# Kernel optimization log

Hardware: AMD Instinct MI355X
Metric: run time of the kernel (lower is better)

Reference implementation:

```python
import jax, jax.numpy as jnp
import numpy as np

N_LAYERS = 2
N_ENT = 50000


def setup_inputs() -> dict:
    key = jax.random.key(0)
    k1, k2, k3, k4, k5 = jax.random.split(key, 5)
    R, N, D, E = 16, N_ENT, 128, 50000
    return {
        "ent_emb": jax.random.normal(k1, (N, D), dtype=jnp.float32),
        "rel_trans": jax.random.normal(k2, (R, D, D), dtype=jnp.float32) * (1.0 / np.sqrt(D)),
        "edge_val": jax.random.uniform(k3, (R, E), dtype=jnp.float32),
        "edge_row": jax.random.randint(k4, (R, E), 0, N, dtype=jnp.int32),
        "edge_col": jax.random.randint(k5, (R, E), 0, N, dtype=jnp.int32),
    }


def _spmm(row, col, val, emb):
    # out[i] = sum_{edges e with row[e]==i} val[e] * emb[col[e]]  (A @ emb)
    msgs = emb[col] * val[:, None]            # [E, d]
    return jax.ops.segment_sum(msgs, row, num_segments=N_ENT)  # [N, d]


def reference(ent_emb, rel_trans, edge_val, edge_row, edge_col):
    emb = ent_emb
    for _ in range(N_LAYERS):
        # per-relation sparse A_r @ emb -> [R, N, d]
        emb_acc = jax.vmap(_spmm, in_axes=(0, 0, 0, None))(edge_row, edge_col, edge_val, emb)
        # batched relation transform: rel_trans[r] @ emb_acc[r].T, transposed back
        tmp = jnp.einsum("rij,rnj->rni", rel_trans, emb_acc)  # [R, N, d]
        emb = jax.nn.relu(jnp.sum(tmp, axis=0))               # [N, d]
    # F.normalize: L2 along dim=1 with eps=1e-12
    norm = jnp.linalg.norm(emb, axis=1, keepdims=True)
    emb = emb / jnp.maximum(norm, 1e-12)
    return emb
```

## Files before the change

### kernel.cpp

```cpp
#include <hip/hip_runtime.h>
#include <stdint.h>

#define NE 50000
#define DD 128
#define RR 16
#define EE 50000
#define NT 32
#define NTOT (RR * NE)
#define SCAN_BLK 4096
#define NSCAN ((NTOT + SCAN_BLK - 1) / SCAN_BLK)

typedef short  shortx8 __attribute__((ext_vector_type(8)));
typedef short  shortx4 __attribute__((ext_vector_type(4)));
typedef float  floatx4 __attribute__((ext_vector_type(4)));

__device__ __forceinline__ unsigned short f2bf(float f) {
    unsigned u = __float_as_uint(f);
    u += 0x7fffu + ((u >> 16) & 1u);
    return (unsigned short)(u >> 16);
}
__device__ __forceinline__ float bf2f(unsigned short h) {
    return __uint_as_float(((unsigned)h) << 16);
}

#define ZB 782
#define TB 128
#define EB 6250
__global__ void prep_k(const float* __restrict__ rt, unsigned short* __restrict__ Tf,
                       const float4* __restrict__ emb, shortx4* __restrict__ embA,
                       int* __restrict__ counts) {
    int b = blockIdx.x, t = threadIdx.x;
    if (b < ZB) {
        int i4 = b * 256 + t;
        if (i4 < NTOT / 4) *(int4*)(counts + i4 * 4) = make_int4(0, 0, 0, 0);
    } else if (b < ZB + TB) {
        int c = (b - ZB) * 256 + t;
        int r = c >> 11, row = (c >> 4) & 127, cb = c & 15;
        int kt = cb >> 2, qq = cb & 3, rg = row >> 4, m = row & 15;
        const float4* src = (const float4*)(rt + (size_t)c * 8);
        float4 v0 = src[0], v1 = src[1];
        shortx8 w;
        w[0] = (short)f2bf(v0.x); w[1] = (short)f2bf(v0.y);
        w[2] = (short)f2bf(v0.z); w[3] = (short)f2bf(v0.w);
        w[4] = (short)f2bf(v1.x); w[5] = (short)f2bf(v1.y);
        w[6] = (short)f2bf(v1.z); w[7] = (short)f2bf(v1.w);
        size_t idx = ((((size_t)r * 8 + rg) * 4 + kt) * 64 + qq * 16 + m) * 8;
        *(shortx8*)(Tf + idx) = w;
    } else {
        int i = (b - ZB - TB) * 256 + t;
        if (i < NE * DD / 4) {
            float4 v = emb[i];
            shortx4 w;
            w[0] = (short)f2bf(v.x); w[1] = (short)f2bf(v.y);
            w[2] = (short)f2bf(v.z); w[3] = (short)f2bf(v.w);
            embA[i] = w;
        }
    }
}

__global__ void hist_k(const int* __restrict__ erow, int* __restrict__ counts,
                       uchar4* __restrict__ rank) {
    int r  = blockIdx.y;
    int i4 = blockIdx.x * 256 + threadIdx.x;
    if (i4 < EE / 4) {
        int4 rw = *(const int4*)(erow + (size_t)r * EE + i4 * 4);
        uchar4 rk;
        rk.x = (unsigned char)atomicAdd(&counts[rw.x * RR + r], 1);
        rk.y = (unsigned char)atomicAdd(&counts[rw.y * RR + r], 1);
        rk.z = (unsigned char)atomicAdd(&counts[rw.z * RR + r], 1);
        rk.w = (unsigned char)atomicAdd(&counts[rw.w * RR + r], 1);
        rank[(size_t)r * (EE / 4) + i4] = rk;
    }
}

__global__ void scanA(const int* __restrict__ c, int* __restrict__ bsum) {
    int b = blockIdx.x, t = threadIdx.x;
    int base = b * SCAN_BLK + t * 16;
    int s = 0;
    #pragma unroll
    for (int i = 0; i < 16; i++) {
        int idx = base + i;
        if (idx < NTOT) s += c[idx];
    }
    __shared__ int sh[256];
    sh[t] = s;
    __syncthreads();
    for (int off = 128; off > 0; off >>= 1) {
        if (t < off) sh[t] += sh[t + off];
        __syncthreads();
    }
    if (t == 0) bsum[b] = sh[0];
}

__global__ void scanC(const int* __restrict__ counts, int* __restrict__ rp,
                      const int* __restrict__ bsum) {
    int b = blockIdx.x, t = threadIdx.x;
    __shared__ int shb[256];
    shb[t] = (t < NSCAN) ? bsum[t] : 0;
    __syncthreads();
    for (int off = 1; off < 256; off <<= 1) {
        int add = (t >= off) ? shb[t - off] : 0;
        __syncthreads();
        shb[t] += add;
        __syncthreads();
    }
    int blockPrefix = (b > 0) ? shb[b - 1] : 0;
    int base = b * SCAN_BLK + t * 16;
    int vals[16];
    int s = 0;
    #pragma unroll
    for (int i = 0; i < 16; i++) {
        int idx = base + i;
        vals[i] = (idx < NTOT) ? counts[idx] : 0;
        s += vals[i];
    }
    __shared__ int sh[256];
    sh[t] = s;
    __syncthreads();
    for (int off = 1; off < 256; off <<= 1) {
        int add = (t >= off) ? sh[t - off] : 0;
        __syncthreads();
        sh[t] += add;
        __syncthreads();
    }
    int run = blockPrefix + sh[t] - s;
    #pragma unroll
    for (int i = 0; i < 16; i++) {
        int idx = base + i;
        if (idx < NTOT) {
            rp[idx] = run;
            run += vals[i];
            if (idx == NTOT - 1) rp[NTOT] = run;
        }
    }
}

__global__ void fill_k(const int* __restrict__ erow, const int* __restrict__ ecol,
                       const float* __restrict__ eval, const int* __restrict__ rp,
                       const uchar4* __restrict__ rank, int2* __restrict__ edges) {
    int r  = blockIdx.y;
    int i4 = blockIdx.x * 256 + threadIdx.x;
    if (i4 < EE / 4) {
        int4   rw = *(const int4*)(erow + (size_t)r * EE + i4 * 4);
        int4   cl = *(const int4*)(ecol + (size_t)r * EE + i4 * 4);
        float4 vl = *(const float4*)(eval + (size_t)r * EE + i4 * 4);
        uchar4 rk = rank[(size_t)r * (EE / 4) + i4];
        edges[rp[rw.x * RR + r] + rk.x] = make_int2(cl.x, __float_as_int(vl.x));
        edges[rp[rw.y * RR + r] + rk.y] = make_int2(cl.y, __float_as_int(vl.y));
        edges[rp[rw.z * RR + r] + rk.z] = make_int2(cl.z, __float_as_int(vl.z));
        edges[rp[rw.w * RR + r] + rk.w] = make_int2(cl.w, __float_as_int(vl.w));
    }
}

__device__ __forceinline__ void accum_chunks(float a0[8], float a1[8], float v,
                                             shortx8 c0, shortx8 c1) {
    #pragma unroll
    for (int j = 0; j < 8; j++) {
        a0[j] = fmaf(v, bf2f((unsigned short)c0[j]), a0[j]);
        a1[j] = fmaf(v, bf2f((unsigned short)c1[j]), a1[j]);
    }
}

template<bool FINAL>
__global__ __launch_bounds__(256, 6)
void layer_k(const unsigned short* __restrict__ embIn,
             const unsigned short* __restrict__ Tf,
             const int* __restrict__ rp,
             const int2* __restrict__ eg,
             unsigned short* __restrict__ embOut,
             float* __restrict__ outF)
{
    __shared__ __align__(16) unsigned short Bt[32 * 128];
    __shared__ float ssred[4][32];

    const int t    = threadIdx.x;
    const int lane = t & 63;
    const int w    = t >> 6;
    const int colq = lane & 15;
    const int q    = lane >> 4;
    const int n0   = blockIdx.x * NT;
    const int nsub = t >> 3;
    const int dgrp = t & 7;

    floatx4 acc[2][2];
    #pragma unroll
    for (int a = 0; a < 2; a++)
        #pragma unroll
        for (int c = 0; c < 2; c++)
            acc[a][c] = (floatx4){0.f, 0.f, 0.f, 0.f};

    #pragma unroll 1
    for (int r = 0; r < RR; r++) {
        int n = n0 + nsub;
        bool ok = n < NE;
        int key = (ok ? n : 0) * RR + r;
        int a = rp[key], b2 = rp[key + 1];
        int s_ = a, c_ = ok ? (b2 - a) : 0;

        int2 E0 = eg[s_];
        int2 E1 = eg[s_ + 1];
        int   col0 = c_ > 0 ? E0.x : 0;
        int   col1 = c_ > 1 ? E1.x : 0;
        float v0_  = c_ > 0 ? __int_as_float(E0.y) : 0.f;
        float v1_  = c_ > 1 ? __int_as_float(E1.y) : 0.f;

        const unsigned short* r0 = embIn + (size_t)col0 * DD + dgrp * 8;
        const unsigned short* r1 = embIn + (size_t)col1 * DD + dgrp * 8;
        shortx8 m00 = *(const shortx8*)r0;
        shortx8 m01 = *(const shortx8*)(r0 + 64);
        shortx8 m10 = *(const shortx8*)r1;
        shortx8 m11 = *(const shortx8*)(r1 + 64);

        float a0[8], a1[8];
        #pragma unroll
        for (int j = 0; j < 8; j++) { a0[j] = 0.f; a1[j] = 0.f; }
        accum_chunks(a0, a1, v0_, m00, m01);
        accum_chunks(a0, a1, v1_, m10, m11);
        if (c_ > 2) {
            #pragma unroll 1
            for (int k = s_ + 2; k < s_ + c_; k++) {
                int2 E = eg[k];
                float v = __int_as_float(E.y);
                const unsigned short* rw_ = embIn + (size_t)E.x * DD + dgrp * 8;
                accum_chunks(a0, a1, v, *(const shortx8*)rw_, *(const shortx8*)(rw_ + 64));
            }
        }
        shortx8 w0, w1;
        #pragma unroll
        for (int j = 0; j < 8; j++) { w0[j] = (short)f2bf(a0[j]); w1[j] = (short)f2bf(a1[j]); }
        int pc = (dgrp ^ nsub) & 7;
        *(shortx8*)&Bt[nsub * 128 + pc * 8] = w0;
        *(shortx8*)&Bt[nsub * 128 + (8 | pc) * 8] = w1;
        __syncthreads();

        shortx8 afN[2];
        #pragma unroll
        for (int it2 = 0; it2 < 2; it2++)
            afN[it2] = *(const shortx8*)(Tf + ((((size_t)r * 8 + (w * 2 + it2)) * 4 + 0) * 64 + lane) * 8);
        #pragma unroll 1
        for (int kt = 0; kt < 4; kt++) {
            shortx8 afC[2];
            afC[0] = afN[0]; afC[1] = afN[1];
            if (kt < 3) {
                #pragma unroll
                for (int it2 = 0; it2 < 2; it2++)
                    afN[it2] = *(const shortx8*)(Tf + ((((size_t)r * 8 + (w * 2 + it2)) * 4 + (kt + 1)) * 64 + lane) * 8);
            }
            int lc = kt * 4 + q;
            shortx8 bfr[2];
            #pragma unroll
            for (int c = 0; c < 2; c++) {
                int nl = c * 16 + colq;
                int pcr = (lc & 8) | ((lc ^ nl) & 7);
                bfr[c] = *(const shortx8*)&Bt[nl * 128 + pcr * 8];
            }
            #pragma unroll
            for (int it2 = 0; it2 < 2; it2++)
                #pragma unroll
                for (int c = 0; c < 2; c++)
                    acc[it2][c] = __builtin_amdgcn_mfma_f32_16x16x32_bf16(afC[it2], bfr[c], acc[it2][c], 0, 0, 0);
        }
        __syncthreads();
    }

    if (!FINAL) {
        #pragma unroll
        for (int c = 0; c < 2; c++) {
            int n = n0 + c * 16 + colq;
            if (n < NE) {
                #pragma unroll
                for (int it2 = 0; it2 < 2; it2++) {
                    shortx4 wv;
                    #pragma unroll
                    for (int g = 0; g < 4; g++) {
                        float v = acc[it2][c][g];
                        v = v > 0.f ? v : 0.f;
                        wv[g] = (short)f2bf(v);
                    }
                    *(shortx4*)(embOut + ((size_t)n * DD + w * 32 + it2 * 16 + q * 4)) = wv;
                }
            }
        }
    } else {
        #pragma unroll
        for (int c = 0; c < 2; c++) {
            float ss = 0.f;
            #pragma unroll
            for (int it2 = 0; it2 < 2; it2++)
                #pragma unroll
                for (int g = 0; g < 4; g++) {
                    float v = acc[it2][c][g];
                    v = v > 0.f ? v : 0.f;
                    acc[it2][c][g] = v;
                    ss += v * v;
                }
            ss += __shfl_xor(ss, 16, 64);
            ss += __shfl_xor(ss, 32, 64);
            if (q == 0) ssred[w][c * 16 + colq] = ss;
        }
        __syncthreads();
        #pragma unroll
        for (int c = 0; c < 2; c++) {
            int nl = c * 16 + colq;
            float tot = ssred[0][nl] + ssred[1][nl] + ssred[2][nl] + ssred[3][nl];
            float scale = 1.f / fmaxf(sqrtf(tot), 1e-12f);
            int n = n0 + nl;
            if (n < NE) {
                #pragma unroll
                for (int it2 = 0; it2 < 2; it2++) {
                    floatx4 v4;
                    #pragma unroll
                    for (int g = 0; g < 4; g++) v4[g] = acc[it2][c][g] * scale;
                    *(floatx4*)(outF + ((size_t)n * DD + w * 32 + it2 * 16 + q * 4)) = v4;
                }
            }
        }
    }
}

static inline size_t align256(size_t x) { return (x + 255) & ~(size_t)255; }

extern "C" void kernel_launch(void* const* d_in, const int* in_sizes, int n_in,
                              void* d_out, int out_size, void* d_ws, size_t ws_size,
                              hipStream_t stream)
{
    const float* ent_emb   = (const float*)d_in[0];
    const float* rel_trans = (const float*)d_in[1];
    const float* edge_val  = (const float*)d_in[2];
    const int*   edge_row  = (const int*)d_in[3];
    const int*   edge_col  = (const int*)d_in[4];
    float* out = (float*)d_out;

    char* ws = (char*)d_ws;
    size_t off = 0;
    int* counts = (int*)(ws + off);  off = align256(off + (size_t)NTOT * 4);
    int* rpf    = (int*)(ws + off);  off = align256(off + ((size_t)NTOT + 1) * 4);
    int* bsum   = (int*)(ws + off);  off = align256(off + 256 * 4);
    uchar4* rank = (uchar4*)(ws + off); off = align256(off + (size_t)NTOT);
    int2* edges = (int2*)(ws + off); off = align256(off + ((size_t)NTOT + 4) * 8);
    unsigned short* Tf   = (unsigned short*)(ws + off); off = align256(off + (size_t)RR * DD * DD * 2);
    unsigned short* embA = (unsigned short*)(ws + off); off = align256(off + (size_t)NE * DD * 2);
    unsigned short* embB = (unsigned short*)(ws + off); off = align256(off + (size_t)NE * DD * 2);

    prep_k<<<ZB + TB + EB, 256, 0, stream>>>(rel_trans, Tf, (const float4*)ent_emb,
                                             (shortx4*)embA, counts);
    dim3 eg_grid((EE / 4 + 255) / 256, RR);
    hist_k<<<eg_grid, 256, 0, stream>>>(edge_row, counts, rank);
    scanA<<<NSCAN, 256, 0, stream>>>(counts, bsum);
    scanC<<<NSCAN, 256, 0, stream>>>(counts, rpf, bsum);
    fill_k<<<eg_grid, 256, 0, stream>>>(edge_row, edge_col, edge_val, rpf, rank, edges);

    int nb = (NE + NT - 1) / NT;
    layer_k<false><<<nb, 256, 0, stream>>>(embA, Tf, rpf, edges, embB, nullptr);
    layer_k<true ><<<nb, 256, 0, stream>>>(embB, Tf, rpf, edges, nullptr, out);
}
```

Before: 363.4 us.

## Switch CSR to relation-major order and gather edges per block via LDS atomics

The CSR key order changes from node-major to relation-major, so each block's edges for one relation form a single contiguous range. Each edge also carries its local node index packed into the upper bits of the column. The gather phase now spreads edges evenly across the 32 node slots, with one edge per 8-thread group, and accumulates into a float LDS tile using shared-memory atomics. This removes the load imbalance from per-node loops over uneven edge counts, but it adds LDS float atomics, a per-relation zeroing pass with an extra barrier, and a larger LDS footprint that may reduce occupancy.

```diff
diff --git a/kernel.cpp b/kernel.cpp
--- a/kernel.cpp
+++ b/kernel.cpp
@@ -64,11 +64,12 @@
     int i4 = blockIdx.x * 256 + threadIdx.x;
     if (i4 < EE / 4) {
         int4 rw = *(const int4*)(erow + (size_t)r * EE + i4 * 4);
+        int base0 = r * NE;
         uchar4 rk;
-        rk.x = (unsigned char)atomicAdd(&counts[rw.x * RR + r], 1);
-        rk.y = (unsigned char)atomicAdd(&counts[rw.y * RR + r], 1);
-        rk.z = (unsigned char)atomicAdd(&counts[rw.z * RR + r], 1);
-        rk.w = (unsigned char)atomicAdd(&counts[rw.w * RR + r], 1);
+        rk.x = (unsigned char)atomicAdd(&counts[base0 + rw.x], 1);
+        rk.y = (unsigned char)atomicAdd(&counts[base0 + rw.y], 1);
+        rk.z = (unsigned char)atomicAdd(&counts[base0 + rw.z], 1);
+        rk.w = (unsigned char)atomicAdd(&counts[base0 + rw.w], 1);
         rank[(size_t)r * (EE / 4) + i4] = rk;
     }
 }
@@ -145,19 +146,11 @@
         int4   cl = *(const int4*)(ecol + (size_t)r * EE + i4 * 4);
         float4 vl = *(const float4*)(eval + (size_t)r * EE + i4 * 4);
         uchar4 rk = rank[(size_t)r * (EE / 4) + i4];
-        edges[rp[rw.x * RR + r] + rk.x] = make_int2(cl.x, __float_as_int(vl.x));
-        edges[rp[rw.y * RR + r] + rk.y] = make_int2(cl.y, __float_as_int(vl.y));
-        edges[rp[rw.z * RR + r] + rk.z] = make_int2(cl.z, __float_as_int(vl.z));
-        edges[rp[rw.w * RR + r] + rk.w] = make_int2(cl.w, __float_as_int(vl.w));
-    }
-}
-
-__device__ __forceinline__ void accum_chunks(float a0[8], float a1[8], float v,
-                                             shortx8 c0, shortx8 c1) {
-    #pragma unroll
-    for (int j = 0; j < 8; j++) {
-        a0[j] = fmaf(v, bf2f((unsigned short)c0[j]), a0[j]);
-        a1[j] = fmaf(v, bf2f((unsigned short)c1[j]), a1[j]);
+        int base0 = r * NE;
+        edges[rp[base0 + rw.x] + rk.x] = make_int2(((rw.x & 31) << 17) | cl.x, __float_as_int(vl.x));
+        edges[rp[base0 + rw.y] + rk.y] = make_int2(((rw.y & 31) << 17) | cl.y, __float_as_int(vl.y));
+        edges[rp[base0 + rw.z] + rk.z] = make_int2(((rw.z & 31) << 17) | cl.z, __float_as_int(vl.z));
+        edges[rp[base0 + rw.w] + rk.w] = make_int2(((rw.w & 31) << 17) | cl.w, __float_as_int(vl.w));
     }
 }
 
@@ -170,6 +163,7 @@
              unsigned short* __restrict__ embOut,
              float* __restrict__ outF)
 {
+    __shared__ float BtF[32 * 132];
     __shared__ __align__(16) unsigned short Bt[32 * 128];
     __shared__ float ssred[4][32];
 
@@ -179,8 +173,9 @@
     const int colq = lane & 15;
     const int q    = lane >> 4;
     const int n0   = blockIdx.x * NT;
-    const int nsub = t >> 3;
+    const int node = t >> 3;
     const int dgrp = t & 7;
+    const int nhi  = (NE - n0 < NT) ? (NE - n0) : NT;
 
     floatx4 acc[2][2];
     #pragma unroll
@@ -191,46 +186,57 @@
 
     #pragma unroll 1
     for (int r = 0; r < RR; r++) {
-        int n = n0 + nsub;
-        bool ok = n < NE;
-        int key = (ok ? n : 0) * RR + r;
-        int a = rp[key], b2 = rp[key + 1];
-        int s_ = a, c_ = ok ? (b2 - a) : 0;
-
-        int2 E0 = eg[s_];
-        int2 E1 = eg[s_ + 1];
-        int   col0 = c_ > 0 ? E0.x : 0;
-        int   col1 = c_ > 1 ? E1.x : 0;
-        float v0_  = c_ > 0 ? __int_as_float(E0.y) : 0.f;
-        float v1_  = c_ > 1 ? __int_as_float(E1.y) : 0.f;
-
-        const unsigned short* r0 = embIn + (size_t)col0 * DD + dgrp * 8;
-        const unsigned short* r1 = embIn + (size_t)col1 * DD + dgrp * 8;
-        shortx8 m00 = *(const shortx8*)r0;
-        shortx8 m01 = *(const shortx8*)(r0 + 64);
-        shortx8 m10 = *(const shortx8*)r1;
-        shortx8 m11 = *(const shortx8*)(r1 + 64);
-
-        float a0[8], a1[8];
-        #pragma unroll
-        for (int j = 0; j < 8; j++) { a0[j] = 0.f; a1[j] = 0.f; }
-        accum_chunks(a0, a1, v0_, m00, m01);
-        accum_chunks(a0, a1, v1_, m10, m11);
-        if (c_ > 2) {
-            #pragma unroll 1
-            for (int k = s_ + 2; k < s_ + c_; k++) {
-                int2 E = eg[k];
-                float v = __int_as_float(E.y);
-                const unsigned short* rw_ = embIn + (size_t)E.x * DD + dgrp * 8;
-                accum_chunks(a0, a1, v, *(const shortx8*)rw_, *(const shortx8*)(rw_ + 64));
-            }
-        }
-        shortx8 w0, w1;
-        #pragma unroll
-        for (int j = 0; j < 8; j++) { w0[j] = (short)f2bf(a0[j]); w1[j] = (short)f2bf(a1[j]); }
-        int pc = (dgrp ^ nsub) & 7;
-        *(shortx8*)&Bt[nsub * 128 + pc * 8] = w0;
-        *(shortx8*)&Bt[nsub * 128 + (8 | pc) * 8] = w1;
+        #pragma unroll
+        for (int i = 0; i < 17; i++) {
+            int idx = t + i * 256;
+            if (idx < 32 * 132) BtF[idx] = 0.f;
+        }
+        __syncthreads();
+
+        int kb = r * NE + n0;
+        int lo = rp[kb];
+        int hi = rp[kb + nhi];
+        int ER = hi - lo;
+        #pragma unroll 1
+        for (int base = 0; base < ER; base += 32) {
+            int ei = base + node;
+            bool ok = ei < ER;
+            int2 E = eg[lo + ei];
+            int   x = ok ? E.x : 0;
+            float v = ok ? __int_as_float(E.y) : 0.f;
+            int nl  = (x >> 17) & 31;
+            int col = x & 0x1FFFF;
+            const unsigned short* rowp = embIn + (size_t)col * DD + dgrp * 16;
+            shortx8 c0 = *(const shortx8*)rowp;
+            shortx8 c1 = *(const shortx8*)(rowp + 8);
+            if (ok) {
+                float* dst = &BtF[nl * 132 + dgrp * 16];
+                #pragma unroll
+                for (int j = 0; j < 8; j++) atomicAdd(&dst[j],     v * bf2f((unsigned short)c0[j]));
+                #pragma unroll
+                for (int j = 0; j < 8; j++) atomicAdd(&dst[8 + j], v * bf2f((unsigned short)c1[j]));
+            }
+        }
+        __syncthreads();
+
+        {
+            const float* src = &BtF[node * 132 + dgrp * 8];
+            floatx4 f0 = *(const floatx4*)(src);
+            floatx4 f1 = *(const floatx4*)(src + 4);
+            floatx4 f2 = *(const floatx4*)(src + 64);
+            floatx4 f3 = *(const floatx4*)(src + 68);
+            shortx8 w0, w1;
+            #pragma unroll
+            for (int j = 0; j < 4; j++) {
+                w0[j]     = (short)f2bf(f0[j]);
+                w0[4 + j] = (short)f2bf(f1[j]);
+                w1[j]     = (short)f2bf(f2[j]);
+                w1[4 + j] = (short)f2bf(f3[j]);
+            }
+            int pc = (dgrp ^ node) & 7;
+            *(shortx8*)&Bt[node * 128 + pc * 8] = w0;
+            *(shortx8*)&Bt[node * 128 + (8 | pc) * 8] = w1;
+        }
         __syncthreads();
 
         shortx8 afN[2];
@@ -260,7 +266,6 @@
                 for (int c = 0; c < 2; c++)
                     acc[it2][c] = __builtin_amdgcn_mfma_f32_16x16x32_bf16(afC[it2], bfr[c], acc[it2][c], 0, 0, 0);
         }
-        __syncthreads();
     }
 
     if (!FINAL) {
@@ -282,6 +287,7 @@
             }
         }
     } else {
+        __syncthreads();
         #pragma unroll
         for (int c = 0; c < 2; c++) {
             float ss = 0.f;
@@ -337,7 +343,7 @@
     int* rpf    = (int*)(ws + off);  off = align256(off + ((size_t)NTOT + 1) * 4);
     int* bsum   = (int*)(ws + off);  off = align256(off + 256 * 4);
     uchar4* rank = (uchar4*)(ws + off); off = align256(off + (size_t)NTOT);
-    int2* edges = (int2*)(ws + off); off = align256(off + ((size_t)NTOT + 4) * 8);
+    int2* edges = (int2*)(ws + off); off = align256(off + ((size_t)NTOT + 32) * 8);
     unsigned short* Tf   = (unsigned short*)(ws + off); off = align256(off + (size_t)RR * DD * DD * 2);
     unsigned short* embA = (unsigned short*)(ws + off); off = align256(off + (size_t)NE * DD * 2);
     unsigned short* embB = (unsigned short*)(ws + off); off = align256(off + (size_t)NE * DD * 2);
```

Measured after the change: 1.440 ms. 3.96x slower.

## Double node tile to 64 with 512 threads and 8 waves per output slice

Applied to the files above, without the earlier changes.

Each block now handles 64 nodes with 512 threads, and each of 8 waves owns a 16-row slice of the output dimension instead of 4 waves with 32 rows. A wave loads one transform fragment per k-step and reuses it across four node column groups, so each fragment is loaded once per 64 nodes instead of once per 32. The edge loop also prefetches the next edge record one iteration ahead, and the edge buffer padding grows to cover that read past the end. Larger blocks halve the block count and raise per-block LDS and register demand, which may cut occupancy and lengthen the per-relation barriers.

```diff
diff --git a/kernel.cpp b/kernel.cpp
--- a/kernel.cpp
+++ b/kernel.cpp
@@ -5,7 +5,7 @@
 #define DD 128
 #define RR 16
 #define EE 50000
-#define NT 32
+#define NT 64
 #define NTOT (RR * NE)
 #define SCAN_BLK 4096
 #define NSCAN ((NTOT + SCAN_BLK - 1) / SCAN_BLK)
@@ -162,7 +162,7 @@
 }
 
 template<bool FINAL>
-__global__ __launch_bounds__(256, 6)
+__global__ __launch_bounds__(512, 6)
 void layer_k(const unsigned short* __restrict__ embIn,
              const unsigned short* __restrict__ Tf,
              const int* __restrict__ rp,
@@ -170,8 +170,8 @@
              unsigned short* __restrict__ embOut,
              float* __restrict__ outF)
 {
-    __shared__ __align__(16) unsigned short Bt[32 * 128];
-    __shared__ float ssred[4][32];
+    __shared__ __align__(16) unsigned short Bt[64 * 128];
+    __shared__ float ssred[8][64];
 
     const int t    = threadIdx.x;
     const int lane = t & 63;
@@ -182,12 +182,10 @@
     const int nsub = t >> 3;
     const int dgrp = t & 7;
 
-    floatx4 acc[2][2];
-    #pragma unroll
-    for (int a = 0; a < 2; a++)
-        #pragma unroll
-        for (int c = 0; c < 2; c++)
-            acc[a][c] = (floatx4){0.f, 0.f, 0.f, 0.f};
+    floatx4 acc[4];
+    #pragma unroll
+    for (int c = 0; c < 4; c++)
+        acc[c] = (floatx4){0.f, 0.f, 0.f, 0.f};
 
     #pragma unroll 1
     for (int r = 0; r < RR; r++) {
@@ -217,12 +215,14 @@
         accum_chunks(a0, a1, v0_, m00, m01);
         accum_chunks(a0, a1, v1_, m10, m11);
         if (c_ > 2) {
+            int2 Ecur = eg[s_ + 2];
             #pragma unroll 1
             for (int k = s_ + 2; k < s_ + c_; k++) {
-                int2 E = eg[k];
-                float v = __int_as_float(E.y);
-                const unsigned short* rw_ = embIn + (size_t)E.x * DD + dgrp * 8;
+                int2 Enx = eg[k + 1];
+                float v = __int_as_float(Ecur.y);
+                const unsigned short* rw_ = embIn + (size_t)Ecur.x * DD + dgrp * 8;
                 accum_chunks(a0, a1, v, *(const shortx8*)rw_, *(const shortx8*)(rw_ + 64));
+                Ecur = Enx;
             }
         }
         shortx8 w0, w1;
@@ -233,86 +233,71 @@
         *(shortx8*)&Bt[nsub * 128 + (8 | pc) * 8] = w1;
         __syncthreads();
 
-        shortx8 afN[2];
-        #pragma unroll
-        for (int it2 = 0; it2 < 2; it2++)
-            afN[it2] = *(const shortx8*)(Tf + ((((size_t)r * 8 + (w * 2 + it2)) * 4 + 0) * 64 + lane) * 8);
+        shortx8 afN = *(const shortx8*)(Tf + ((((size_t)r * 8 + w) * 4 + 0) * 64 + lane) * 8);
         #pragma unroll 1
         for (int kt = 0; kt < 4; kt++) {
-            shortx8 afC[2];
-            afC[0] = afN[0]; afC[1] = afN[1];
-            if (kt < 3) {
-                #pragma unroll
-                for (int it2 = 0; it2 < 2; it2++)
-                    afN[it2] = *(const shortx8*)(Tf + ((((size_t)r * 8 + (w * 2 + it2)) * 4 + (kt + 1)) * 64 + lane) * 8);
-            }
+            shortx8 afC = afN;
+            if (kt < 3)
+                afN = *(const shortx8*)(Tf + ((((size_t)r * 8 + w) * 4 + (kt + 1)) * 64 + lane) * 8);
             int lc = kt * 4 + q;
-            shortx8 bfr[2];
+            shortx8 bfr[4];
             #pragma unroll
-            for (int c = 0; c < 2; c++) {
+            for (int c = 0; c < 4; c++) {
                 int nl = c * 16 + colq;
                 int pcr = (lc & 8) | ((lc ^ nl) & 7);
                 bfr[c] = *(const shortx8*)&Bt[nl * 128 + pcr * 8];
             }
             #pragma unroll
-            for (int it2 = 0; it2 < 2; it2++)
-                #pragma unroll
-                for (int c = 0; c < 2; c++)
-                    acc[it2][c] = __builtin_amdgcn_mfma_f32_16x16x32_bf16(afC[it2], bfr[c], acc[it2][c], 0, 0, 0);
+            for (int c = 0; c < 4; c++)
+                acc[c] = __builtin_amdgcn_mfma_f32_16x16x32_bf16(afC, bfr[c], acc[c], 0, 0, 0);
         }
         __syncthreads();
     }
 
     if (!FINAL) {
         #pragma unroll
-        for (int c = 0; c < 2; c++) {
+        for (int c = 0; c < 4; c++) {
             int n = n0 + c * 16 + colq;
             if (n < NE) {
+                shortx4 wv;
                 #pragma unroll
-                for (int it2 = 0; it2 < 2; it2++) {
-                    shortx4 wv;
-                    #pragma unroll
-                    for (int g = 0; g < 4; g++) {
-                        float v = acc[it2][c][g];
-                        v = v > 0.f ? v : 0.f;
-                        wv[g] = (short)f2bf(v);
-                    }
-                    *(shortx4*)(embOut + ((size_t)n * DD + w * 32 + it2 * 16 + q * 4)) = wv;
+                for (int g = 0; g < 4; g++) {
+                    float v = acc[c][g];
+                    v = v > 0.f ? v : 0.f;
+                    wv[g] = (short)f2bf(v);
                 }
+                *(shortx4*)(embOut + ((size_t)n * DD + w * 16 + q * 4)) = wv;
             }
         }
     } else {
         #pragma unroll
-        for (int c = 0; c < 2; c++) {
+        for (int c = 0; c < 4; c++) {
             float ss = 0.f;
             #pragma unroll
-            for (int it2 = 0; it2 < 2; it2++)
-                #pragma unroll
-                for (int g = 0; g < 4; g++) {
-                    float v = acc[it2][c][g];
-                    v = v > 0.f ? v : 0.f;
-                    acc[it2][c][g] = v;
-                    ss += v * v;
-                }
+            for (int g = 0; g < 4; g++) {
+                float v = acc[c][g];
+                v = v > 0.f ? v : 0.f;
+                acc[c][g] = v;
+                ss += v * v;
+            }
             ss += __shfl_xor(ss, 16, 64);
             ss += __shfl_xor(ss, 32, 64);
             if (q == 0) ssred[w][c * 16 + colq] = ss;
         }
         __syncthreads();
         #pragma unroll
-        for (int c = 0; c < 2; c++) {
+        for (int c = 0; c < 4; c++) {
             int nl = c * 16 + colq;
-            float tot = ssred[0][nl] + ssred[1][nl] + ssred[2][nl] + ssred[3][nl];
+            float tot = 0.f;
+            #pragma unroll
+            for (int ww = 0; ww < 8; ww++) tot += ssred[ww][nl];
             float scale = 1.f / fmaxf(sqrtf(tot), 1e-12f);
             int n = n0 + nl;
             if (n < NE) {
+                floatx4 v4;
                 #pragma unroll
-                for (int it2 = 0; it2 < 2; it2++) {
-                    floatx4 v4;
-                    #pragma unroll
-                    for (int g = 0; g < 4; g++) v4[g] = acc[it2][c][g] * scale;
-                    *(floatx4*)(outF + ((size_t)n * DD + w * 32 + it2 * 16 + q * 4)) = v4;
-                }
+                for (int g = 0; g < 4; g++) v4[g] = acc[c][g] * scale;
+                *(floatx4*)(outF + ((size_t)n * DD + w * 16 + q * 4)) = v4;
             }
         }
     }
@@ -337,7 +322,7 @@
     int* rpf    = (int*)(ws + off);  off = align256(off + ((size_t)NTOT + 1) * 4);
     int* bsum   = (int*)(ws + off);  off = align256(off + 256 * 4);
     uchar4* rank = (uchar4*)(ws + off); off = align256(off + (size_t)NTOT);
-    int2* edges = (int2*)(ws + off); off = align256(off + ((size_t)NTOT + 4) * 8);
+    int2* edges = (int2*)(ws + off); off = align256(off + ((size_t)NTOT + 8) * 8);
     unsigned short* Tf   = (unsigned short*)(ws + off); off = align256(off + (size_t)RR * DD * DD * 2);
     unsigned short* embA = (unsigned short*)(ws + off); off = align256(off + (size_t)NE * DD * 2);
     unsigned short* embB = (unsigned short*)(ws + off); off = align256(off + (size_t)NE * DD * 2);
@@ -351,6 +336,6 @@
     fill_k<<<eg_grid, 256, 0, stream>>>(edge_row, edge_col, edge_val, rpf, rank, edges);
 
     int nb = (NE + NT - 1) / NT;
-    layer_k<false><<<nb, 256, 0, stream>>>(embA, Tf, rpf, edges, embB, nullptr);
-    layer_k<true ><<<nb, 256, 0, stream>>>(embB, Tf, rpf, edges, nullptr, out);
-}
+    layer_k<false><<<nb, 512, 0, stream>>>(embA, Tf, rpf, edges, embB, nullptr);
+    layer_k<true ><<<nb, 512, 0, stream>>>(embB, Tf, rpf, edges, nullptr, out);
+}
```

After: 384.4 us. 1.06x slower.

## Restructure layer kernel to per-wave node tiles with register-resident B fragments and prefetch

Applied to the files above, without the earlier changes.

Each wave now owns 16 nodes, and each lane gathers one node's neighbor rows directly into the MFMA B-fragment layout. This removes the LDS staging buffer and both __syncthreads per relation. The next relation's edge metadata and first two neighbor rows are prefetched, double-buffered, while the current relation's MFMAs run. The full 128x128 transform is streamed per wave with double-buffered A fragments. The cost is many more registers (occupancy hint lowered to 3) and each wave re-reading the whole transform matrix per relation, which raises L2 traffic.

```diff
diff --git a/kernel.cpp b/kernel.cpp
--- a/kernel.cpp
+++ b/kernel.cpp
@@ -5,7 +5,7 @@
 #define DD 128
 #define RR 16
 #define EE 50000
-#define NT 32
+#define NT 64
 #define NTOT (RR * NE)
 #define SCAN_BLK 4096
 #define NSCAN ((NTOT + SCAN_BLK - 1) / SCAN_BLK)
@@ -152,17 +152,8 @@
     }
 }
 
-__device__ __forceinline__ void accum_chunks(float a0[8], float a1[8], float v,
-                                             shortx8 c0, shortx8 c1) {
-    #pragma unroll
-    for (int j = 0; j < 8; j++) {
-        a0[j] = fmaf(v, bf2f((unsigned short)c0[j]), a0[j]);
-        a1[j] = fmaf(v, bf2f((unsigned short)c1[j]), a1[j]);
-    }
-}
-
 template<bool FINAL>
-__global__ __launch_bounds__(256, 6)
+__global__ __launch_bounds__(256, 3)
 void layer_k(const unsigned short* __restrict__ embIn,
              const unsigned short* __restrict__ Tf,
              const int* __restrict__ rp,
@@ -170,149 +161,152 @@
              unsigned short* __restrict__ embOut,
              float* __restrict__ outF)
 {
-    __shared__ __align__(16) unsigned short Bt[32 * 128];
-    __shared__ float ssred[4][32];
-
     const int t    = threadIdx.x;
     const int lane = t & 63;
-    const int w    = t >> 6;
-    const int colq = lane & 15;
-    const int q    = lane >> 4;
-    const int n0   = blockIdx.x * NT;
-    const int nsub = t >> 3;
-    const int dgrp = t & 7;
-
-    floatx4 acc[2][2];
+    const int wv   = t >> 6;
+    const int nl   = lane & 15;
+    const int qq   = lane >> 4;
+    const int n    = blockIdx.x * NT + wv * 16 + nl;
+    const bool ok  = n < NE;
+    const int key0 = (ok ? n : NE - 1) * RR;
+
+    floatx4 acc[8];
     #pragma unroll
-    for (int a = 0; a < 2; a++)
-        #pragma unroll
-        for (int c = 0; c < 2; c++)
-            acc[a][c] = (floatx4){0.f, 0.f, 0.f, 0.f};
-
-    #pragma unroll 1
-    for (int r = 0; r < RR; r++) {
-        int n = n0 + nsub;
-        bool ok = n < NE;
-        int key = (ok ? n : 0) * RR + r;
-        int a = rp[key], b2 = rp[key + 1];
-        int s_ = a, c_ = ok ? (b2 - a) : 0;
-
-        int2 E0 = eg[s_];
-        int2 E1 = eg[s_ + 1];
-        int   col0 = c_ > 0 ? E0.x : 0;
-        int   col1 = c_ > 1 ? E1.x : 0;
-        float v0_  = c_ > 0 ? __int_as_float(E0.y) : 0.f;
-        float v1_  = c_ > 1 ? __int_as_float(E1.y) : 0.f;
-
-        const unsigned short* r0 = embIn + (size_t)col0 * DD + dgrp * 8;
-        const unsigned short* r1 = embIn + (size_t)col1 * DD + dgrp * 8;
-        shortx8 m00 = *(const shortx8*)r0;
-        shortx8 m01 = *(const shortx8*)(r0 + 64);
-        shortx8 m10 = *(const shortx8*)r1;
-        shortx8 m11 = *(const shortx8*)(r1 + 64);
-
-        float a0[8], a1[8];
-        #pragma unroll
-        for (int j = 0; j < 8; j++) { a0[j] = 0.f; a1[j] = 0.f; }
-        accum_chunks(a0, a1, v0_, m00, m01);
-        accum_chunks(a0, a1, v1_, m10, m11);
-        if (c_ > 2) {
+    for (int i = 0; i < 8; i++) acc[i] = (floatx4){0.f, 0.f, 0.f, 0.f};
+
+    int   sM[2], cM[2];
+    float v0M[2], v1M[2];
+    shortx8 m0[2][4], m1[2][4];
+
+    {
+        int a = rp[key0], b = rp[key0 + 1];
+        int cnt = ok ? (b - a) : 0;
+        sM[0] = a; cM[0] = cnt;
+        int2 E0 = eg[a], E1 = eg[a + 1];
+        int col0 = cnt > 0 ? E0.x : 0;
+        int col1 = cnt > 1 ? E1.x : col0;
+        v0M[0] = cnt > 0 ? __int_as_float(E0.y) : 0.f;
+        v1M[0] = cnt > 1 ? __int_as_float(E1.y) : 0.f;
+        const unsigned short* r0 = embIn + (size_t)col0 * DD + qq * 8;
+        const unsigned short* r1 = embIn + (size_t)col1 * DD + qq * 8;
+        #pragma unroll
+        for (int kt = 0; kt < 4; kt++) {
+            m0[0][kt] = *(const shortx8*)(r0 + kt * 32);
+            m1[0][kt] = *(const shortx8*)(r1 + kt * 32);
+        }
+    }
+
+    auto body = [&](int r, int ph) {
+        const int pn = ph ^ 1;
+        float aS[32];
+        #pragma unroll
+        for (int kt = 0; kt < 4; kt++)
+            #pragma unroll
+            for (int j = 0; j < 8; j++)
+                aS[kt * 8 + j] = fmaf(v0M[ph], bf2f((unsigned short)m0[ph][kt][j]),
+                                      v1M[ph] * bf2f((unsigned short)m1[ph][kt][j]));
+        if (cM[ph] > 2) {
+            int s = sM[ph];
             #pragma unroll 1
-            for (int k = s_ + 2; k < s_ + c_; k++) {
+            for (int k = s + 2; k < s + cM[ph]; k++) {
                 int2 E = eg[k];
                 float v = __int_as_float(E.y);
-                const unsigned short* rw_ = embIn + (size_t)E.x * DD + dgrp * 8;
-                accum_chunks(a0, a1, v, *(const shortx8*)rw_, *(const shortx8*)(rw_ + 64));
-            }
-        }
-        shortx8 w0, w1;
-        #pragma unroll
-        for (int j = 0; j < 8; j++) { w0[j] = (short)f2bf(a0[j]); w1[j] = (short)f2bf(a1[j]); }
-        int pc = (dgrp ^ nsub) & 7;
-        *(shortx8*)&Bt[nsub * 128 + pc * 8] = w0;
-        *(shortx8*)&Bt[nsub * 128 + (8 | pc) * 8] = w1;
-        __syncthreads();
-
-        shortx8 afN[2];
-        #pragma unroll
-        for (int it2 = 0; it2 < 2; it2++)
-            afN[it2] = *(const shortx8*)(Tf + ((((size_t)r * 8 + (w * 2 + it2)) * 4 + 0) * 64 + lane) * 8);
-        #pragma unroll 1
-        for (int kt = 0; kt < 4; kt++) {
-            shortx8 afC[2];
-            afC[0] = afN[0]; afC[1] = afN[1];
-            if (kt < 3) {
+                const unsigned short* rw = embIn + (size_t)E.x * DD + qq * 8;
                 #pragma unroll
-                for (int it2 = 0; it2 < 2; it2++)
-                    afN[it2] = *(const shortx8*)(Tf + ((((size_t)r * 8 + (w * 2 + it2)) * 4 + (kt + 1)) * 64 + lane) * 8);
-            }
-            int lc = kt * 4 + q;
-            shortx8 bfr[2];
-            #pragma unroll
-            for (int c = 0; c < 2; c++) {
-                int nl = c * 16 + colq;
-                int pcr = (lc & 8) | ((lc ^ nl) & 7);
-                bfr[c] = *(const shortx8*)&Bt[nl * 128 + pcr * 8];
-            }
-            #pragma unroll
-            for (int it2 = 0; it2 < 2; it2++)
+                for (int kt = 0; kt < 4; kt++) {
+                    shortx8 mm = *(const shortx8*)(rw + kt * 32);
+                    #pragma unroll
+                    for (int j = 0; j < 8; j++)
+                        aS[kt * 8 + j] = fmaf(v, bf2f((unsigned short)mm[j]), aS[kt * 8 + j]);
+                }
+            }
+        }
+        shortx8 bf[4];
+        #pragma unroll
+        for (int kt = 0; kt < 4; kt++)
+            #pragma unroll
+            for (int j = 0; j < 8; j++)
+                bf[kt][j] = (short)f2bf(aS[kt * 8 + j]);
+
+        if (r < 15) {
+            int a = rp[key0 + r + 1], b = rp[key0 + r + 2];
+            int cnt = ok ? (b - a) : 0;
+            sM[pn] = a; cM[pn] = cnt;
+            int2 E0 = eg[a], E1 = eg[a + 1];
+            int col0 = cnt > 0 ? E0.x : 0;
+            int col1 = cnt > 1 ? E1.x : col0;
+            v0M[pn] = cnt > 0 ? __int_as_float(E0.y) : 0.f;
+            v1M[pn] = cnt > 1 ? __int_as_float(E1.y) : 0.f;
+            const unsigned short* r0 = embIn + (size_t)col0 * DD + qq * 8;
+            const unsigned short* r1 = embIn + (size_t)col1 * DD + qq * 8;
+            #pragma unroll
+            for (int kt = 0; kt < 4; kt++) {
+                m0[pn][kt] = *(const shortx8*)(r0 + kt * 32);
+                m1[pn][kt] = *(const shortx8*)(r1 + kt * 32);
+            }
+        }
+        __builtin_amdgcn_sched_barrier(0);
+
+        const unsigned short* tb = Tf + (size_t)r * 8 * 4 * 64 * 8;
+        shortx8 af[2][4];
+        #pragma unroll
+        for (int kt = 0; kt < 4; kt++)
+            af[0][kt] = *(const shortx8*)(tb + ((size_t)(0 * 4 + kt) * 64 + lane) * 8);
+        #pragma unroll
+        for (int tt = 0; tt < 8; tt++) {
+            const int cur = tt & 1, nxt = cur ^ 1;
+            if (tt < 7) {
                 #pragma unroll
-                for (int c = 0; c < 2; c++)
-                    acc[it2][c] = __builtin_amdgcn_mfma_f32_16x16x32_bf16(afC[it2], bfr[c], acc[it2][c], 0, 0, 0);
-        }
-        __syncthreads();
+                for (int kt = 0; kt < 4; kt++)
+                    af[nxt][kt] = *(const shortx8*)(tb + ((size_t)((tt + 1) * 4 + kt) * 64 + lane) * 8);
+            }
+            #pragma unroll
+            for (int kt = 0; kt < 4; kt++)
+                acc[tt] = __builtin_amdgcn_mfma_f32_16x16x32_bf16(af[cur][kt], bf[kt], acc[tt], 0, 0, 0);
+        }
+    };
+
+    #pragma unroll 1
+    for (int h = 0; h < 8; h++) {
+        body(2 * h,     0);
+        body(2 * h + 1, 1);
     }
 
     if (!FINAL) {
-        #pragma unroll
-        for (int c = 0; c < 2; c++) {
-            int n = n0 + c * 16 + colq;
-            if (n < NE) {
-                #pragma unroll
-                for (int it2 = 0; it2 < 2; it2++) {
-                    shortx4 wv;
-                    #pragma unroll
-                    for (int g = 0; g < 4; g++) {
-                        float v = acc[it2][c][g];
-                        v = v > 0.f ? v : 0.f;
-                        wv[g] = (short)f2bf(v);
-                    }
-                    *(shortx4*)(embOut + ((size_t)n * DD + w * 32 + it2 * 16 + q * 4)) = wv;
-                }
-            }
-        }
-    } else {
-        #pragma unroll
-        for (int c = 0; c < 2; c++) {
-            float ss = 0.f;
-            #pragma unroll
-            for (int it2 = 0; it2 < 2; it2++)
+        if (ok) {
+            #pragma unroll
+            for (int tt = 0; tt < 8; tt++) {
+                shortx4 wvx;
                 #pragma unroll
                 for (int g = 0; g < 4; g++) {
-                    float v = acc[it2][c][g];
+                    float v = acc[tt][g];
                     v = v > 0.f ? v : 0.f;
-                    acc[it2][c][g] = v;
-                    ss += v * v;
+                    wvx[g] = (short)f2bf(v);
                 }
-            ss += __shfl_xor(ss, 16, 64);
-            ss += __shfl_xor(ss, 32, 64);
-            if (q == 0) ssred[w][c * 16 + colq] = ss;
-        }
-        __syncthreads();
-        #pragma unroll
-        for (int c = 0; c < 2; c++) {
-            int nl = c * 16 + colq;
-            float tot = ssred[0][nl] + ssred[1][nl] + ssred[2][nl] + ssred[3][nl];
-            float scale = 1.f / fmaxf(sqrtf(tot), 1e-12f);
-            int n = n0 + nl;
-            if (n < NE) {
+                *(shortx4*)(embOut + ((size_t)n * DD + tt * 16 + qq * 4)) = wvx;
+            }
+        }
+    } else {
+        float ss = 0.f;
+        #pragma unroll
+        for (int tt = 0; tt < 8; tt++)
+            #pragma unroll
+            for (int g = 0; g < 4; g++) {
+                float v = acc[tt][g];
+                v = v > 0.f ? v : 0.f;
+                acc[tt][g] = v;
+                ss += v * v;
+            }
+        ss += __shfl_xor(ss, 16, 64);
+        ss += __shfl_xor(ss, 32, 64);
+        float scale = 1.f / fmaxf(sqrtf(ss), 1e-12f);
+        if (ok) {
+            #pragma unroll
+            for (int tt = 0; tt < 8; tt++) {
+                floatx4 v4;
                 #pragma unroll
-                for (int it2 = 0; it2 < 2; it2++) {
-                    floatx4 v4;
-                    #pragma unroll
-                    for (int g = 0; g < 4; g++) v4[g] = acc[it2][c][g] * scale;
-                    *(floatx4*)(outF + ((size_t)n * DD + w * 32 + it2 * 16 + q * 4)) = v4;
-                }
+                for (int g = 0; g < 4; g++) v4[g] = acc[tt][g] * scale;
+                *(floatx4*)(outF + ((size_t)n * DD + tt * 16 + qq * 4)) = v4;
             }
         }
     }
@@ -337,7 +331,7 @@
     int* rpf    = (int*)(ws + off);  off = align256(off + ((size_t)NTOT + 1) * 4);
     int* bsum   = (int*)(ws + off);  off = align256(off + 256 * 4);
     uchar4* rank = (uchar4*)(ws + off); off = align256(off + (size_t)NTOT);
-    int2* edges = (int2*)(ws + off); off = align256(off + ((size_t)NTOT + 4) * 8);
+    int2* edges = (int2*)(ws + off); off = align256(off + ((size_t)NTOT + 8) * 8);
     unsigned short* Tf   = (unsigned short*)(ws + off); off = align256(off + (size_t)RR * DD * DD * 2);
     unsigned short* embA = (unsigned short*)(ws + off); off = align256(off + (size_t)NE * DD * 2);
     unsigned short* embB = (unsigned short*)(ws + off); off = align256(off + (size_t)NE * DD * 2);
```

Result: slower. 538.9 us (+48.3%).
